# Kernel optimization log

Hardware: AMD Instinct MI355X
Metric: run time of the kernel (lower is better)

Reference implementation:

```python
import jax, jax.numpy as jnp
import numpy as np

B, S, H = 2, 2048, 2048
NH, NKV, HD = 16, 4, 128
SCALING = HD ** -0.5


def rotate_half(x):
    x1, x2 = jnp.split(x, 2, axis=-1)
    return jnp.concatenate((-x2, x1), axis=-1)


def apply_rope(t, cos, sin):
    # t: [B, nh, S, HD]; cos/sin: [B, S, HD] -> unsqueeze head dim
    c = cos[:, None, :, :]
    s = sin[:, None, :, :]
    return t * c + rotate_half(t) * s


def setup_inputs() -> dict:
    key = jax.random.key(0)
    k1, k2, k3, k4, k5 = jax.random.split(key, 5)
    hidden_states = jax.random.normal(k1, (B, S, H), dtype=jnp.float32)
    # real RoPE tables
    inv_freq = 1.0 / (10000.0 ** (jnp.arange(0, HD, 2, dtype=jnp.float32) / HD))
    pos = jnp.arange(S, dtype=jnp.float32)
    freqs = jnp.einsum('s,d->sd', pos, inv_freq)              # [S, HD/2]
    emb = jnp.concatenate((freqs, freqs), axis=-1)            # [S, HD]
    cos = jnp.broadcast_to(jnp.cos(emb)[None], (B, S, HD))
    sin = jnp.broadcast_to(jnp.sin(emb)[None], (B, S, HD))
    # additive causal mask [B, 1, S, S]
    causal = jnp.triu(jnp.full((S, S), -1e9, dtype=jnp.float32), k=1)
    attention_mask = jnp.broadcast_to(causal[None, None], (B, 1, S, S))
    sc = 0.02
    wq = jax.random.normal(k2, (NH * HD, H), dtype=jnp.float32) * sc
    wk = jax.random.normal(k3, (NKV * HD, H), dtype=jnp.float32) * sc
    wv = jax.random.normal(k4, (NKV * HD, H), dtype=jnp.float32) * sc
    wo = jax.random.normal(k5, (H, NH * HD), dtype=jnp.float32) * sc
    return {"hidden_states": hidden_states, "cos": cos, "sin": sin,
            "attention_mask": attention_mask, "wq": wq, "wk": wk, "wv": wv, "wo": wo}


def reference(hidden_states, cos, sin, attention_mask, wq, wk, wv, wo):
    x = hidden_states
    # fused-style QKV projections (nn.Linear: x @ W.T), split heads -> [B, nh, S, HD]
    q = (x @ wq.T).reshape(B, S, NH, HD).transpose(0, 2, 1, 3)
    k = (x @ wk.T).reshape(B, S, NKV, HD).transpose(0, 2, 1, 3)
    v = (x @ wv.T).reshape(B, S, NKV, HD).transpose(0, 2, 1, 3)
    q = apply_rope(q, cos, sin)
    k = apply_rope(k, cos, sin)
    # GQA: repeat KV heads (repeat_kv)
    n_rep = NH // NKV
    k = jnp.repeat(k, n_rep, axis=1)
    v = jnp.repeat(v, n_rep, axis=1)
    scores = jnp.einsum('bhqd,bhkd->bhqk', q, k) * SCALING + attention_mask
    attn = jax.nn.softmax(scores.astype(jnp.float32), axis=-1).astype(q.dtype)
    out = jnp.einsum('bhqk,bhkd->bhqd', attn, v)
    out = out.transpose(0, 2, 1, 3).reshape(B, S, NH * HD)
    out = out @ wo.T
    return (out, attn)
```

## Files before the change

kernel.cpp:

```cpp
#include <hip/hip_runtime.h>
#include <cstdint>
#include <cstddef>

typedef __bf16 bf16;
typedef __attribute__((ext_vector_type(8))) __bf16 bf16x8;
typedef __attribute__((ext_vector_type(4))) __bf16 bf16x4;
typedef __attribute__((ext_vector_type(4))) float f32x4;

constexpr int B_ = 2, S_ = 2048, H_ = 2048, NH_ = 16, NKV_ = 4, HD_ = 128;
constexpr float SCALE_ = 0.08838834764831845f;

#define GLDS16(g, l)                                                        \
  __builtin_amdgcn_global_load_lds(                                         \
      (const __attribute__((address_space(1))) void*)(g),                   \
      (__attribute__((address_space(3))) void*)(l), 16, 0, 0)

#define VMCNT0 asm volatile("s_waitcnt vmcnt(0)" ::: "memory")
#define VMCNT4 asm volatile("s_waitcnt vmcnt(4)" ::: "memory")
#define BAR __builtin_amdgcn_s_barrier()

__global__ void cvt_all(const float* __restrict__ hs, const float* __restrict__ wq,
                        const float* __restrict__ wk, const float* __restrict__ wv,
                        const float* __restrict__ wo, bf16* __restrict__ xb,
                        bf16* __restrict__ w3b, bf16* __restrict__ wob) {
  const int stride = gridDim.x * blockDim.x;
  for (int i = blockIdx.x * blockDim.x + threadIdx.x; i < 4718592; i += stride) {
    const float4* s; bf16x4* d; int j;
    if (i < 2097152)      { s = (const float4*)hs; d = (bf16x4*)xb;            j = i; }
    else if (i < 3145728) { s = (const float4*)wq; d = (bf16x4*)w3b;           j = i - 2097152; }
    else if (i < 3407872) { s = (const float4*)wk; d = (bf16x4*)w3b + 1048576; j = i - 3145728; }
    else if (i < 3670016) { s = (const float4*)wv; d = (bf16x4*)w3b + 1310720; j = i - 3407872; }
    else                  { s = (const float4*)wo; d = (bf16x4*)wob;           j = i - 3670016; }
    float4 v = s[j];
    bf16x4 o;
    o[0] = (bf16)v.x; o[1] = (bf16)v.y; o[2] = (bf16)v.z; o[3] = (bf16)v.w;
    d[j] = o;
  }
}

template <int EPI>
__global__ __launch_bounds__(256, 2) void gemm_bt(const bf16* __restrict__ A,
                                                  const bf16* __restrict__ Bm, int K,
                                                  bf16* __restrict__ qb, bf16* __restrict__ kb,
                                                  bf16* __restrict__ vtb, float* __restrict__ Cout) {
  __shared__ __align__(16) bf16 As[2][128 * 64];
  __shared__ __align__(16) bf16 Bs[2][128 * 64];
  const int tid = threadIdx.x;
  const int lane = tid & 63;
  const int wid = tid >> 6;
  const int fid = blockIdx.y * 32 + blockIdx.x;
  const int nwg = gridDim.y * 32;
  const int swz = (fid & 7) * (nwg >> 3) + (fid >> 3);
  const int m0 = (swz & 31) * 128;
  const int n0 = (swz >> 5) * 128;
  const int wm = (wid >> 1) * 64, wn = (wid & 1) * 64;
  const int r = lane & 15, g = lane >> 4;
  f32x4 acc[4][4] = {};

  auto STAGE = [&](int kt, int cc) {
#pragma unroll
    for (int i = 0; i < 4; ++i) {
      int cb = wid * 256 + i * 64;
      int c64 = cb + lane;
      int row = c64 >> 3, cs = (c64 & 7) ^ (row & 7);
      GLDS16(A + (size_t)(m0 + row) * K + kt + cs * 8, &As[cc][cb * 8]);
      GLDS16(Bm + (size_t)(n0 + row) * K + kt + cs * 8, &Bs[cc][cb * 8]);
    }
  };

  STAGE(0, 0);
  VMCNT0; BAR;
  int c = 0;
#pragma unroll 1
  for (int kt = 0; kt < K; kt += 64) {
    if (kt + 64 < K) STAGE(kt + 64, c ^ 1);
#pragma unroll
    for (int ks = 0; ks < 2; ++ks) {
      bf16x8 af[4], bfr[4];
#pragma unroll
      for (int fm = 0; fm < 4; ++fm)
        af[fm] = *(const bf16x8*)(&As[c][(wm + fm * 16 + r) * 64 + (((ks * 4 + g) ^ (r & 7)) << 3)]);
#pragma unroll
      for (int fn = 0; fn < 4; ++fn)
        bfr[fn] = *(const bf16x8*)(&Bs[c][(wn + fn * 16 + r) * 64 + (((ks * 4 + g) ^ (r & 7)) << 3)]);
#pragma unroll
      for (int fm = 0; fm < 4; ++fm)
#pragma unroll
        for (int fn = 0; fn < 4; ++fn)
          acc[fm][fn] = __builtin_amdgcn_mfma_f32_16x16x32_bf16(af[fm], bfr[fn], acc[fm][fn], 0, 0, 0);
    }
    VMCNT0; BAR;
    c ^= 1;
  }

#pragma unroll
  for (int fm = 0; fm < 4; ++fm)
#pragma unroll
    for (int fn = 0; fn < 4; ++fn)
#pragma unroll
      for (int rr = 0; rr < 4; ++rr) {
        int mm = m0 + wm + fm * 16 + g * 4 + rr;
        int nn = n0 + wn + fn * 16 + r;
        float v = acc[fm][fn][rr];
        if (EPI == 1) {
          Cout[(size_t)mm * 2048 + nn] = v;
        } else {
          int b = mm >> 11, s = mm & (S_ - 1);
          int d = nn & 127;
          if (nn < 2048) {
            int hh = nn >> 7;
            qb[(((size_t)b * NH_ + hh) * S_ + s) * HD_ + d] = (bf16)v;
          } else if (nn < 2560) {
            int hh = (nn - 2048) >> 7;
            kb[(((size_t)b * NKV_ + hh) * S_ + s) * HD_ + d] = (bf16)v;
          } else {
            int hh = (nn - 2560) >> 7;
            vtb[(((size_t)b * NKV_ + hh) * HD_ + d) * S_ + s] = (bf16)v;
          }
        }
      }
}

__global__ void rope_kernel(bf16* __restrict__ qb, bf16* __restrict__ kb,
                            const float* __restrict__ cosp, const float* __restrict__ sinp) {
  const int NQ = B_ * NH_ * S_;
  const int NK = B_ * NKV_ * S_;
  int tot = (NQ + NK) * 64;
  for (int t = blockIdx.x * blockDim.x + threadIdx.x; t < tot; t += gridDim.x * blockDim.x) {
    int d = t & 63;
    int rid = t >> 6;
    bf16* base;
    int b, s;
    if (rid < NQ) {
      base = qb + (size_t)rid * HD_;
      s = rid & (S_ - 1);
      b = rid >> 15;
    } else {
      int r2 = rid - NQ;
      base = kb + (size_t)r2 * HD_;
      s = r2 & (S_ - 1);
      b = r2 >> 13;
    }
    float c = cosp[((size_t)b * S_ + s) * HD_ + d];
    float sn = sinp[((size_t)b * S_ + s) * HD_ + d];
    float x1 = (float)base[d], x2 = (float)base[d + 64];
    base[d] = (bf16)(x1 * c - x2 * sn);
    base[d + 64] = (bf16)(x2 * c + x1 * sn);
  }
}

__global__ __launch_bounds__(256, 2) void attn_kernel(const bf16* __restrict__ qb,
                                                      const bf16* __restrict__ kb,
                                                      const bf16* __restrict__ vtb,
                                                      bf16* __restrict__ aob,
                                                      float* __restrict__ attn_out) {
  __shared__ __align__(16) bf16 Ks[2][64 * 128];
  __shared__ __align__(16) bf16 Vs[2][128 * 64];
  __shared__ __align__(16) bf16 Ps[64 * 64];
  const int bid = (blockIdx.x & 7) * 64 + (blockIdx.x >> 3);
  const int p = bid & 15;
  const int h = (bid >> 4) & 15;
  const int b = bid >> 8;
  const int kh = h >> 2;
  const int tid = threadIdx.x, lane = tid & 63, wid = tid >> 6;
  const int r = lane & 15, g = lane >> 4;

  const bf16* kbase = kb + ((size_t)b * NKV_ + kh) * S_ * HD_;
  const bf16* vbase = vtb + ((size_t)b * NKV_ + kh) * (size_t)HD_ * S_;
  const size_t ahead = (size_t)(b * NH_ + h) * S_;

  auto stageK = [&](int kt, int cc) {
#pragma unroll
    for (int i = 0; i < 4; ++i) {
      int base = i * 256 + wid * 64;
      int idx = base + lane;
      int row = idx >> 4, ch = (idx & 15) ^ (row & 7);
      GLDS16(kbase + (size_t)(kt * 64 + row) * HD_ + ch * 8, &Ks[cc][base * 8]);
    }
  };
  auto stageV = [&](int kt, int cc) {
#pragma unroll
    for (int i = 0; i < 4; ++i) {
      int base = i * 256 + wid * 64;
      int idx = base + lane;
      int row = idx >> 3, ch = (idx & 7) ^ (row & 7);
      GLDS16(vbase + (size_t)row * S_ + kt * 64 + ch * 8, &Vs[cc][base * 8]);
    }
  };

  int zc = 0;

#pragma unroll 1
  for (int sbi = 0; sbi < 2; ++sbi) {
    const int qt = sbi ? 31 - p : p;
    const int q0 = qt * 64;
    const int nt = qt + 1;
    const bf16* qsrc = qb + ((size_t)(b * NH_ + h) * S_ + q0) * HD_;

    bf16x8 qreg[4];
#pragma unroll
    for (int ks = 0; ks < 4; ++ks)
      qreg[ks] = *(const bf16x8*)(qsrc + (wid * 16 + r) * HD_ + ks * 32 + g * 8);

    float lsum = 0.f;
    stageK(0, 0);
    VMCNT0; BAR;
    int c = 0;
#pragma unroll 1
    for (int kt = 0; kt < nt; ++kt) {
      if (kt + 1 < nt) stageK(kt + 1, c ^ 1);
      const bool dz = (zc <= 30);
      if (dz) {
        int qtz, ktz;
        if (zc < 31 - p) { qtz = p; ktz = p + 1 + zc; }
        else             { qtz = 31 - p; ktz = zc + 1; }
        float* zdst = attn_out + (ahead + qtz * 64) * S_ + ktz * 64;
        float4 z = {0.f, 0.f, 0.f, 0.f};
#pragma unroll
        for (int i = 0; i < 4; ++i) {
          int idx = i * 256 + tid;
          *(float4*)(zdst + (size_t)(idx >> 4) * S_ + (idx & 15) * 4) = z;
        }
        ++zc;
      }
      f32x4 sacc[4] = {};
      __builtin_amdgcn_s_setprio(1);
#pragma unroll
      for (int ks = 0; ks < 4; ++ks)
#pragma unroll
        for (int fn = 0; fn < 4; ++fn) {
          bf16x8 kk = *(const bf16x8*)(&Ks[c][(fn * 16 + r) * 128 + (((ks * 4 + g) ^ (r & 7)) << 3)]);
          sacc[fn] = __builtin_amdgcn_mfma_f32_16x16x32_bf16(kk, qreg[ks], sacc[fn], 0, 0, 0);
        }
      __builtin_amdgcn_s_setprio(0);
      float ts = 0.f;
      if (kt == nt - 1) {
#pragma unroll
        for (int fn = 0; fn < 4; ++fn)
#pragma unroll
          for (int rr = 0; rr < 4; ++rr) {
            bool msk = (fn * 16 + g * 4 + rr) > (wid * 16 + r);
            ts += msk ? 0.f : __expf(sacc[fn][rr] * SCALE_);
          }
      } else {
#pragma unroll
        for (int fn = 0; fn < 4; ++fn)
#pragma unroll
          for (int rr = 0; rr < 4; ++rr) ts += __expf(sacc[fn][rr] * SCALE_);
      }
      ts += __shfl_xor(ts, 16);
      ts += __shfl_xor(ts, 32);
      lsum += ts;
      if (dz) { VMCNT4; } else { VMCNT0; }
      BAR;
      c ^= 1;
    }
    const float rl = 1.0f / lsum;

    f32x4 oacc[8] = {};
    const size_t arow0 = (ahead + q0) * S_;
    stageK(0, 0);
    stageV(0, 0);
    VMCNT0; BAR;
    c = 0;
#pragma unroll 1
    for (int kt = 0; kt < nt; ++kt) {
      if (kt + 1 < nt) { stageK(kt + 1, c ^ 1); stageV(kt + 1, c ^ 1); }
      const int k0 = kt * 64;
      f32x4 sacc[4] = {};
      __builtin_amdgcn_s_setprio(1);
#pragma unroll
      for (int ks = 0; ks < 4; ++ks)
#pragma unroll
        for (int fn = 0; fn < 4; ++fn) {
          bf16x8 kk = *(const bf16x8*)(&Ks[c][(fn * 16 + r) * 128 + (((ks * 4 + g) ^ (r & 7)) << 3)]);
          sacc[fn] = __builtin_amdgcn_mfma_f32_16x16x32_bf16(kk, qreg[ks], sacc[fn], 0, 0, 0);
        }
      __builtin_amdgcn_s_setprio(0);
      const int prow = (wid * 16 + r) * 64;
      if (kt == nt - 1) {
#pragma unroll
        for (int fn = 0; fn < 4; ++fn) {
          bf16x4 pk;
#pragma unroll
          for (int rr = 0; rr < 4; ++rr) {
            bool msk = (fn * 16 + g * 4 + rr) > (wid * 16 + r);
            pk[rr] = (bf16)(msk ? 0.f : __expf(sacc[fn][rr] * SCALE_) * rl);
          }
          *(bf16x4*)(&Ps[prow + ((((fn << 1) | (g >> 1)) ^ (r & 7)) << 3) + ((g & 1) << 2)]) = pk;
        }
      } else {
#pragma unroll
        for (int fn = 0; fn < 4; ++fn) {
          bf16x4 pk;
#pragma unroll
          for (int rr = 0; rr < 4; ++rr)
            pk[rr] = (bf16)(__expf(sacc[fn][rr] * SCALE_) * rl);
          *(bf16x4*)(&Ps[prow + ((((fn << 1) | (g >> 1)) ^ (r & 7)) << 3) + ((g & 1) << 2)]) = pk;
        }
      }
      {
        const int trow = tid >> 2, tcb = (tid & 3) * 16;
        float* dst = attn_out + arow0 + (size_t)trow * S_ + k0 + tcb;
        int ch0 = (tid & 3) * 2;
        bf16x8 p0 = *(const bf16x8*)(&Ps[trow * 64 + ((ch0 ^ (trow & 7)) << 3)]);
        bf16x8 p1 = *(const bf16x8*)(&Ps[trow * 64 + (((ch0 + 1) ^ (trow & 7)) << 3)]);
        float4 o0 = {(float)p0[0], (float)p0[1], (float)p0[2], (float)p0[3]};
        float4 o1 = {(float)p0[4], (float)p0[5], (float)p0[6], (float)p0[7]};
        float4 o2 = {(float)p1[0], (float)p1[1], (float)p1[2], (float)p1[3]};
        float4 o3 = {(float)p1[4], (float)p1[5], (float)p1[6], (float)p1[7]};
        *(float4*)(dst) = o0;
        *(float4*)(dst + 4) = o1;
        *(float4*)(dst + 8) = o2;
        *(float4*)(dst + 12) = o3;
      }
      __builtin_amdgcn_s_setprio(1);
#pragma unroll
      for (int ks = 0; ks < 2; ++ks) {
        bf16x8 pa = *(const bf16x8*)(&Ps[prow + (((ks * 4 + g) ^ (r & 7)) << 3)]);
#pragma unroll
        for (int fn = 0; fn < 8; ++fn) {
          bf16x8 vv = *(const bf16x8*)(&Vs[c][(fn * 16 + r) * 64 + (((ks * 4 + g) ^ (r & 7)) << 3)]);
          oacc[fn] = __builtin_amdgcn_mfma_f32_16x16x32_bf16(pa, vv, oacc[fn], 0, 0, 0);
        }
      }
      __builtin_amdgcn_s_setprio(0);
      VMCNT4; BAR;
      c ^= 1;
    }

#pragma unroll
    for (int fn = 0; fn < 8; ++fn)
#pragma unroll
      for (int rr = 0; rr < 4; ++rr) {
        int q = q0 + wid * 16 + g * 4 + rr;
        aob[((size_t)b * S_ + q) * 2048 + h * HD_ + fn * 16 + r] = (bf16)oacc[fn][rr];
      }
  }
}

extern "C" void kernel_launch(void* const* d_in, const int* in_sizes, int n_in,
                              void* d_out, int out_size, void* d_ws, size_t ws_size,
                              hipStream_t stream) {
  const float* hidden = (const float*)d_in[0];
  const float* cosp = (const float*)d_in[1];
  const float* sinp = (const float*)d_in[2];
  const float* wq = (const float*)d_in[4];
  const float* wk = (const float*)d_in[5];
  const float* wv = (const float*)d_in[6];
  const float* wo = (const float*)d_in[7];
  float* out = (float*)d_out;
  float* attn = out + (size_t)B_ * S_ * H_;

  char* ws = (char*)d_ws;
  bf16* xb  = (bf16*)(ws);
  bf16* w3b = (bf16*)(ws + (16ull << 20));
  bf16* wob = (bf16*)(ws + (28ull << 20));
  bf16* qb  = (bf16*)(ws + (36ull << 20));
  bf16* kb  = (bf16*)(ws + (52ull << 20));
  bf16* vtb = (bf16*)(ws + (56ull << 20));
  bf16* aob = (bf16*)(ws + (60ull << 20));

  cvt_all<<<2048, 256, 0, stream>>>(hidden, wq, wk, wv, wo, xb, w3b, wob);
  gemm_bt<0><<<dim3(32, 24), 256, 0, stream>>>(xb, w3b, 2048, qb, kb, vtb, nullptr);
  rope_kernel<<<2048, 256, 0, stream>>>(qb, kb, cosp, sinp);
  attn_kernel<<<512, 256, 0, stream>>>(qb, kb, vtb, aob, attn);
  gemm_bt<1><<<dim3(32, 16), 256, 0, stream>>>(aob, wob, 2048, nullptr, nullptr, nullptr, out);
}
```

Measured before the change: 353.8 us.

## Use 8-wave 256-row GEMM tiles with phased MFMA and priority scheduling

Replaces the 4-wave 128x128 projection GEMM with an 8-wave kernel using 256xBN tiles (BN=256 for QKV, 128 for output). B fragments are held in registers across the k-step and A is loaded in phases. Each phase is separated by barriers with setprio raised around the MFMA bursts. The aim is more operand reuse per LDS load and better overlap across waves, at the cost of fewer workgroups (192 for QKV, below the CU count) and larger LDS use per block.

Measured after the change: 381.7 us. 7.9% more time.

```diff
diff --git a/kernel.cpp b/kernel.cpp
--- a/kernel.cpp
+++ b/kernel.cpp
@@ -17,6 +17,11 @@
 
 #define VMCNT0 asm volatile("s_waitcnt vmcnt(0)" ::: "memory")
 #define VMCNT4 asm volatile("s_waitcnt vmcnt(4)" ::: "memory")
+#define LGKM0_SB                                                            \
+  do {                                                                      \
+    asm volatile("s_waitcnt lgkmcnt(0)" ::: "memory");                      \
+    __builtin_amdgcn_sched_barrier(0);                                      \
+  } while (0)
 #define BAR __builtin_amdgcn_s_barrier()
 
 __global__ void cvt_all(const float* __restrict__ hs, const float* __restrict__ wq,
@@ -38,69 +43,95 @@
   }
 }
 
-template <int EPI>
-__global__ __launch_bounds__(256, 2) void gemm_bt(const bf16* __restrict__ A,
-                                                  const bf16* __restrict__ Bm, int K,
-                                                  bf16* __restrict__ qb, bf16* __restrict__ kb,
-                                                  bf16* __restrict__ vtb, float* __restrict__ Cout) {
-  __shared__ __align__(16) bf16 As[2][128 * 64];
-  __shared__ __align__(16) bf16 Bs[2][128 * 64];
+template <int BN, int EPI>
+__global__ __launch_bounds__(512, 2) void gemm8(const bf16* __restrict__ A,
+                                                const bf16* __restrict__ Bm, int K,
+                                                bf16* __restrict__ qb, bf16* __restrict__ kb,
+                                                bf16* __restrict__ vtb, float* __restrict__ Cout) {
+  constexpr int FN = BN / 64;
+  constexpr int FMP = (BN == 256) ? 2 : 4;
+  constexpr int PH = 8 / FMP;
+  constexpr int RB = BN / 64;
+  __shared__ __align__(16) bf16 As[2][256 * 64];
+  __shared__ __align__(16) bf16 Bs[2][BN * 64];
   const int tid = threadIdx.x;
   const int lane = tid & 63;
   const int wid = tid >> 6;
-  const int fid = blockIdx.y * 32 + blockIdx.x;
-  const int nwg = gridDim.y * 32;
+  const int wr = wid >> 2, wc = wid & 3;
+  const int r = lane & 15, g = lane >> 4;
+  const int fid = blockIdx.y * gridDim.x + blockIdx.x;
+  const int nwg = gridDim.y * gridDim.x;
   const int swz = (fid & 7) * (nwg >> 3) + (fid >> 3);
-  const int m0 = (swz & 31) * 128;
-  const int n0 = (swz >> 5) * 128;
-  const int wm = (wid >> 1) * 64, wn = (wid & 1) * 64;
-  const int r = lane & 15, g = lane >> 4;
-  f32x4 acc[4][4] = {};
+  const int m0 = (swz & 15) << 8;
+  const int n0 = (swz >> 4) * BN;
+
+  f32x4 acc[8][FN] = {};
 
   auto STAGE = [&](int kt, int cc) {
 #pragma unroll
-    for (int i = 0; i < 4; ++i) {
-      int cb = wid * 256 + i * 64;
-      int c64 = cb + lane;
-      int row = c64 >> 3, cs = (c64 & 7) ^ (row & 7);
-      GLDS16(A + (size_t)(m0 + row) * K + kt + cs * 8, &As[cc][cb * 8]);
-      GLDS16(Bm + (size_t)(n0 + row) * K + kt + cs * 8, &Bs[cc][cb * 8]);
+    for (int j = 0; j < 4; ++j) {
+      int base = j * 512 + wid * 64;
+      int idx = base + lane;
+      int row = idx >> 3, ch = (idx & 7) ^ (row & 7);
+      GLDS16(A + (size_t)(m0 + row) * K + kt + ch * 8, &As[cc][base * 8]);
+    }
+#pragma unroll
+    for (int j = 0; j < RB; ++j) {
+      int base = j * 512 + wid * 64;
+      int idx = base + lane;
+      int row = idx >> 3, ch = (idx & 7) ^ (row & 7);
+      GLDS16(Bm + (size_t)(n0 + row) * K + kt + ch * 8, &Bs[cc][base * 8]);
     }
   };
 
   STAGE(0, 0);
   VMCNT0; BAR;
-  int c = 0;
+  int cur = 0;
 #pragma unroll 1
   for (int kt = 0; kt < K; kt += 64) {
-    if (kt + 64 < K) STAGE(kt + 64, c ^ 1);
-#pragma unroll
-    for (int ks = 0; ks < 2; ++ks) {
-      bf16x8 af[4], bfr[4];
-#pragma unroll
-      for (int fm = 0; fm < 4; ++fm)
-        af[fm] = *(const bf16x8*)(&As[c][(wm + fm * 16 + r) * 64 + (((ks * 4 + g) ^ (r & 7)) << 3)]);
-#pragma unroll
-      for (int fn = 0; fn < 4; ++fn)
-        bfr[fn] = *(const bf16x8*)(&Bs[c][(wn + fn * 16 + r) * 64 + (((ks * 4 + g) ^ (r & 7)) << 3)]);
-#pragma unroll
-      for (int fm = 0; fm < 4; ++fm)
-#pragma unroll
-        for (int fn = 0; fn < 4; ++fn)
-          acc[fm][fn] = __builtin_amdgcn_mfma_f32_16x16x32_bf16(af[fm], bfr[fn], acc[fm][fn], 0, 0, 0);
-    }
-    VMCNT0; BAR;
-    c ^= 1;
+    if (kt + 64 < K) STAGE(kt + 64, cur ^ 1);
+    bf16x8 bfr[FN][2];
+#pragma unroll
+    for (int fn = 0; fn < FN; ++fn)
+#pragma unroll
+      for (int ks = 0; ks < 2; ++ks)
+        bfr[fn][ks] = *(const bf16x8*)(&Bs[cur][(wc * (FN * 16) + fn * 16 + r) * 64 +
+                                                (((ks * 4 + g) ^ (r & 7)) << 3)]);
+#pragma unroll
+    for (int p = 0; p < PH; ++p) {
+      bf16x8 af[FMP][2];
+#pragma unroll
+      for (int i = 0; i < FMP; ++i)
+#pragma unroll
+        for (int ks = 0; ks < 2; ++ks)
+          af[i][ks] = *(const bf16x8*)(&As[cur][(wr * 128 + (p * FMP + i) * 16 + r) * 64 +
+                                                (((ks * 4 + g) ^ (r & 7)) << 3)]);
+      BAR;
+      LGKM0_SB;
+      __builtin_amdgcn_s_setprio(1);
+#pragma unroll
+      for (int i = 0; i < FMP; ++i)
+#pragma unroll
+        for (int fn = 0; fn < FN; ++fn)
+#pragma unroll
+          for (int ks = 0; ks < 2; ++ks)
+            acc[p * FMP + i][fn] = __builtin_amdgcn_mfma_f32_16x16x32_bf16(
+                af[i][ks], bfr[fn][ks], acc[p * FMP + i][fn], 0, 0, 0);
+      __builtin_amdgcn_s_setprio(0);
+      if (p == PH - 1 && kt + 64 < K) { VMCNT0; }
+      BAR;
+    }
+    cur ^= 1;
   }
 
 #pragma unroll
-  for (int fm = 0; fm < 4; ++fm)
-#pragma unroll
-    for (int fn = 0; fn < 4; ++fn)
+  for (int fm = 0; fm < 8; ++fm)
+#pragma unroll
+    for (int fn = 0; fn < FN; ++fn)
 #pragma unroll
       for (int rr = 0; rr < 4; ++rr) {
-        int mm = m0 + wm + fm * 16 + g * 4 + rr;
-        int nn = n0 + wn + fn * 16 + r;
+        int mm = m0 + wr * 128 + fm * 16 + g * 4 + rr;
+        int nn = n0 + wc * (FN * 16) + fn * 16 + r;
         float v = acc[fm][fn][rr];
         if (EPI == 1) {
           Cout[(size_t)mm * 2048 + nn] = v;
@@ -362,8 +393,8 @@
   bf16* aob = (bf16*)(ws + (60ull << 20));
 
   cvt_all<<<2048, 256, 0, stream>>>(hidden, wq, wk, wv, wo, xb, w3b, wob);
-  gemm_bt<0><<<dim3(32, 24), 256, 0, stream>>>(xb, w3b, 2048, qb, kb, vtb, nullptr);
+  gemm8<256, 0><<<dim3(16, 12), 512, 0, stream>>>(xb, w3b, 2048, qb, kb, vtb, nullptr);
   rope_kernel<<<2048, 256, 0, stream>>>(qb, kb, cosp, sinp);
   attn_kernel<<<512, 256, 0, stream>>>(qb, kb, vtb, aob, attn);
-  gemm_bt<1><<<dim3(32, 16), 256, 0, stream>>>(aob, wob, 2048, nullptr, nullptr, nullptr, out);
+  gemm8<128, 1><<<dim3(16, 16), 512, 0, stream>>>(aob, wob, 2048, nullptr, nullptr, nullptr, out);
 }
```
